# Kernel optimization log

Hardware: AMD Instinct MI355X
Metric: run time of the kernel (lower is better)

The kernel has to match this reference:

```python
import jax, jax.numpy as jnp
import numpy as np
import math

N_HEADS, INPUT_DIM, EMBED_DIM = 8, 512, 512
KEY_DIM = EMBED_DIM // N_HEADS  # val_dim == key_dim == 64
B, NQ, G = 4, 2048, 2048


def setup_inputs() -> dict:
    key = jax.random.key(0)
    ks = jax.random.split(key, 7)
    stdv_k = 1.0 / math.sqrt(KEY_DIM)
    stdv_e = 1.0 / math.sqrt(EMBED_DIM)
    return {
        "q": jax.random.normal(ks[0], (B, NQ, INPUT_DIM), jnp.float32),
        "h": jax.random.normal(ks[1], (B, G, INPUT_DIM), jnp.float32),
        "mask": jax.random.randint(ks[2], (B, NQ, G), 0, 2) == 1,  # True = attention not possible
        "W_query": jax.random.uniform(ks[3], (N_HEADS, INPUT_DIM, KEY_DIM), jnp.float32, -stdv_k, stdv_k),
        "W_key": jax.random.uniform(ks[4], (N_HEADS, INPUT_DIM, KEY_DIM), jnp.float32, -stdv_k, stdv_k),
        "W_val": jax.random.uniform(ks[5], (N_HEADS, INPUT_DIM, KEY_DIM), jnp.float32, -stdv_k, stdv_k),
        "W_out": jax.random.uniform(ks[6], (N_HEADS, KEY_DIM, EMBED_DIM), jnp.float32, -stdv_e, stdv_e),
    }


def reference(q, h, mask, W_query, W_key, W_val, W_out):
    norm = 1.0 / math.sqrt(KEY_DIM)
    # Per-head projections: (H, B, S, kd)
    Q = jnp.einsum("bqd,hdk->hbqk", q, W_query)
    K = jnp.einsum("bgd,hdk->hbgk", h, W_key)
    V = jnp.einsum("bgd,hdv->hbgv", h, W_val)
    # Full attention scores: (H, B, NQ, G)
    comp = norm * jnp.einsum("hbqk,hbgk->hbqg", Q, K)
    m = mask[None]  # (1, B, NQ, G) broadcasts over heads
    comp = jnp.where(m, -jnp.inf, comp)
    attn = jax.nn.softmax(comp, axis=-1)
    attn = jnp.where(m, 0.0, attn)  # mirrors the clone + zero step (also fixes all-masked rows)
    heads = jnp.einsum("hbqg,hbgv->hbqv", attn, V)
    # Output projection: flatten heads and apply W_out (H, vd, E)
    out = jnp.einsum("hbqv,hve->bqe", heads, W_out)
    return out
```

## Files before the change

### kernel.cpp

```cpp
#include <hip/hip_runtime.h>
#include <hip/hip_bf16.h>
#include <stdint.h>

#define NHEADS 8
#define INDIM 512
#define EMB 512
#define BSZ 4
#define NQS 2048
#define GS 2048

#define ALPHA_F 0.18033688011112042f

#if __has_builtin(__builtin_amdgcn_exp2f)
#define EXP2(x) __builtin_amdgcn_exp2f(x)
#else
#define EXP2(x) __expf((x)*0.69314718056f)
#endif

typedef short bf16x8 __attribute__((ext_vector_type(8)));
typedef float f32x4 __attribute__((ext_vector_type(4)));
typedef float f32x16 __attribute__((ext_vector_type(16)));
typedef unsigned int u32x4 __attribute__((ext_vector_type(4)));

static __device__ __forceinline__ unsigned short f2bf(float f) {
  unsigned int u = __builtin_bit_cast(unsigned int, f);
  unsigned int rounding = 0x7FFFu + ((u >> 16) & 1u);
  u += rounding;
  return (unsigned short)(u >> 16);
}

typedef __attribute__((address_space(3))) void lds_void;
typedef __attribute__((address_space(1))) const void gm_void;
static __device__ __forceinline__ void gll16(const void* g, void* s) {
  __builtin_amdgcn_global_load_lds((gm_void*)g, (lds_void*)s, 16, 0, 0);
}

__global__ void k_prep(const float4* __restrict__ q, const float4* __restrict__ h,
                       const void* __restrict__ mask,
                       const float* __restrict__ wq, const float* __restrict__ wk,
                       const float* __restrict__ wv, const float* __restrict__ wo,
                       ushort4* __restrict__ qb, ushort4* __restrict__ hb,
                       unsigned short* __restrict__ wqt, unsigned short* __restrict__ wkvt,
                       unsigned short* __restrict__ wot, unsigned short* __restrict__ maskB16) {
  int blk = blockIdx.x, t = threadIdx.x;
  if (blk < 2048) {
    const float4* src = blk < 1024 ? q : h;
    ushort4* dst = blk < 1024 ? qb : hb;
    int base = (blk & 1023) * 256 + t;
#pragma unroll
    for (int i = 0; i < 4; i++) {
      int idx = base + i * 262144;
      float4 v = src[idx];
      ushort4 o;
      o.x = f2bf(v.x); o.y = f2bf(v.y); o.z = f2bf(v.z); o.w = f2bf(v.w);
      dst[idx] = o;
    }
  } else if (blk < 3072) {
    const unsigned int* m32h = (const unsigned int*)mask;
    bool bytes = __ballot(m32h[t & 63] > 1u) != 0ull;
    int base = (blk - 2048) * 256 + t;
#pragma unroll
    for (int i = 0; i < 4; i++) {
      int widx = base + i * 262144;
      unsigned int bits = 0;
      if (bytes) {
        const uchar4* p = (const uchar4*)((const unsigned char*)mask + (size_t)widx * 16);
#pragma unroll
        for (int j = 0; j < 4; j++) {
          uchar4 v = p[j];
          bits |= ((v.x ? 1u : 0u) << (4 * j)) | ((v.y ? 1u : 0u) << (4 * j + 1)) |
                  ((v.z ? 1u : 0u) << (4 * j + 2)) | ((v.w ? 1u : 0u) << (4 * j + 3));
        }
      } else {
        const int4* p = (const int4*)((const int*)mask + (size_t)widx * 16);
#pragma unroll
        for (int j = 0; j < 4; j++) {
          int4 v = p[j];
          bits |= ((v.x ? 1u : 0u) << (4 * j)) | ((v.y ? 1u : 0u) << (4 * j + 1)) |
                  ((v.z ? 1u : 0u) << (4 * j + 2)) | ((v.w ? 1u : 0u) << (4 * j + 3));
        }
      }
      maskB16[widx] = (unsigned short)bits;
    }
  } else {
    int id = (blk - 3072) * 256 + t;
#pragma unroll
    for (int i = 0; i < 8; i++) {
      int e = id * 8 + i;
      int which = e >> 18, r = e & 262143;
      int k = r & 511, n = r >> 9;
      int hh = n >> 6, j = n & 63;
      if (which == 0) wqt[r] = f2bf(wq[hh * 32768 + k * 64 + j] * ALPHA_F);
      else if (which == 1) wkvt[r] = f2bf(wk[hh * 32768 + k * 64 + j]);
      else if (which == 2) wkvt[262144 + r] = f2bf(wv[hh * 32768 + k * 64 + j]);
      else wot[r] = f2bf(wo[k * 512 + n]);
    }
  }
}

template <int MODE>
__global__ __launch_bounds__(256) void k_gemm3(const unsigned short* __restrict__ A,
                                               const unsigned short* __restrict__ Bt,
                                               void* __restrict__ C, void* __restrict__ C2) {
  __shared__ unsigned short As[2][4096];
  __shared__ unsigned short Bs[2][8192];
  int m0 = blockIdx.x * 64, n0 = blockIdx.y * 128;
  int t = threadIdx.x;
  int w = t >> 6, l = t & 63, c = l & 15, lg = l >> 4;
  int wr = w >> 1, wc = w & 1;

  int rbA = t >> 7, kcc = (t >> 4) & 7, cc = t & 15;
  const unsigned short* aG = A + (size_t)(m0 + rbA * 16 + cc) * 512 + kcc * 8;
  const unsigned short* bG = Bt + (size_t)(n0 + rbA * 16 + cc) * 512 + kcc * 8;
  int ldsOff = w * 1024 + (t & 63) * 16;

  f32x4 acc[2][4];
#pragma unroll
  for (int mi = 0; mi < 2; mi++)
#pragma unroll
    for (int ni = 0; ni < 4; ni++) acc[mi][ni] = {0.f, 0.f, 0.f, 0.f};

  gll16(aG, (char*)As[0] + ldsOff);
  gll16(aG + 32 * 512, (char*)As[0] + ldsOff + 4096);
  gll16(bG, (char*)Bs[0] + ldsOff);
  gll16(bG + 32 * 512, (char*)Bs[0] + ldsOff + 4096);
  gll16(bG + 64 * 512, (char*)Bs[0] + ldsOff + 8192);
  gll16(bG + 96 * 512, (char*)Bs[0] + ldsOff + 12288);

  for (int kk = 0; kk < 8; kk++) {
    int cur = kk & 1;
    asm volatile("s_waitcnt vmcnt(0)" ::: "memory");
    __builtin_amdgcn_s_barrier();
    if (kk < 7) {
      int ko = (kk + 1) * 64;
      gll16(aG + ko, (char*)As[cur ^ 1] + ldsOff);
      gll16(aG + ko + 32 * 512, (char*)As[cur ^ 1] + ldsOff + 4096);
      gll16(bG + ko, (char*)Bs[cur ^ 1] + ldsOff);
      gll16(bG + ko + 32 * 512, (char*)Bs[cur ^ 1] + ldsOff + 4096);
      gll16(bG + ko + 64 * 512, (char*)Bs[cur ^ 1] + ldsOff + 8192);
      gll16(bG + ko + 96 * 512, (char*)Bs[cur ^ 1] + ldsOff + 12288);
    }
    bf16x8 af[2][2], bfr[4][2];
#pragma unroll
    for (int kc = 0; kc < 2; kc++) {
#pragma unroll
      for (int mi = 0; mi < 2; mi++)
        af[mi][kc] = *(const bf16x8*)((const char*)As[cur] + ((wr * 2 + mi) * 128 + (kc * 4 + lg) * 16 + c) * 16);
#pragma unroll
      for (int ni = 0; ni < 4; ni++)
        bfr[ni][kc] = *(const bf16x8*)((const char*)Bs[cur] + ((wc * 4 + ni) * 128 + (kc * 4 + lg) * 16 + c) * 16);
    }
#pragma unroll
    for (int kc = 0; kc < 2; kc++)
#pragma unroll
      for (int mi = 0; mi < 2; mi++)
#pragma unroll
        for (int ni = 0; ni < 4; ni++)
          acc[mi][ni] = __builtin_amdgcn_mfma_f32_16x16x32_bf16(af[mi][kc], bfr[ni][kc], acc[mi][ni], 0, 0, 0);
  }

#pragma unroll
  for (int mi = 0; mi < 2; mi++)
#pragma unroll
    for (int ni = 0; ni < 4; ni++) {
      int row = m0 + wr * 32 + mi * 16 + 4 * lg;
      int col = n0 + wc * 64 + ni * 16 + c;
#pragma unroll
      for (int r = 0; r < 4; r++)
        ((float*)C)[(size_t)(row + r) * 512 + col] = acc[mi][ni][r];
    }
}

__global__ __launch_bounds__(256) void k_gemmQKV(const unsigned short* __restrict__ qb_,
                                                 const unsigned short* __restrict__ hb_,
                                                 const unsigned short* __restrict__ wqt,
                                                 const unsigned short* __restrict__ wkvt,
                                                 unsigned short* __restrict__ Qp,
                                                 unsigned short* __restrict__ Kp,
                                                 unsigned short* __restrict__ Vt) {
  __shared__ unsigned short As[2][4096];
  __shared__ unsigned short Bs[2][8192];
  int ny = blockIdx.y;
  const unsigned short* A = (ny < 4) ? qb_ : hb_;
  const unsigned short* Bt = (ny < 4) ? wqt : wkvt;
  int n0 = (ny < 4) ? ny * 128 : (ny - 4) * 128;
  int m0 = blockIdx.x * 64;
  int t = threadIdx.x;
  int w = t >> 6, l = t & 63, c = l & 15, lg = l >> 4;
  int wr = w >> 1, wc = w & 1;

  int rbA = t >> 7, kcc = (t >> 4) & 7, cc = t & 15;
  const unsigned short* aG = A + (size_t)(m0 + rbA * 16 + cc) * 512 + kcc * 8;
  const unsigned short* bG = Bt + (size_t)(n0 + rbA * 16 + cc) * 512 + kcc * 8;
  int ldsOff = w * 1024 + (t & 63) * 16;

  f32x4 acc[2][4];
#pragma unroll
  for (int mi = 0; mi < 2; mi++)
#pragma unroll
    for (int ni = 0; ni < 4; ni++) acc[mi][ni] = {0.f, 0.f, 0.f, 0.f};

  gll16(aG, (char*)As[0] + ldsOff);
  gll16(aG + 32 * 512, (char*)As[0] + ldsOff + 4096);
  gll16(bG, (char*)Bs[0] + ldsOff);
  gll16(bG + 32 * 512, (char*)Bs[0] + ldsOff + 4096);
  gll16(bG + 64 * 512, (char*)Bs[0] + ldsOff + 8192);
  gll16(bG + 96 * 512, (char*)Bs[0] + ldsOff + 12288);

  for (int kk = 0; kk < 8; kk++) {
    int cur = kk & 1;
    asm volatile("s_waitcnt vmcnt(0)" ::: "memory");
    __builtin_amdgcn_s_barrier();
    if (kk < 7) {
      int ko = (kk + 1) * 64;
      gll16(aG + ko, (char*)As[cur ^ 1] + ldsOff);
      gll16(aG + ko + 32 * 512, (char*)As[cur ^ 1] + ldsOff + 4096);
      gll16(bG + ko, (char*)Bs[cur ^ 1] + ldsOff);
      gll16(bG + ko + 32 * 512, (char*)Bs[cur ^ 1] + ldsOff + 4096);
      gll16(bG + ko + 64 * 512, (char*)Bs[cur ^ 1] + ldsOff + 8192);
      gll16(bG + ko + 96 * 512, (char*)Bs[cur ^ 1] + ldsOff + 12288);
    }
    bf16x8 af[2][2], bfr[4][2];
#pragma unroll
    for (int kc = 0; kc < 2; kc++) {
#pragma unroll
      for (int mi = 0; mi < 2; mi++)
        af[mi][kc] = *(const bf16x8*)((const char*)As[cur] + ((wr * 2 + mi) * 128 + (kc * 4 + lg) * 16 + c) * 16);
#pragma unroll
      for (int ni = 0; ni < 4; ni++)
        bfr[ni][kc] = *(const bf16x8*)((const char*)Bs[cur] + ((wc * 4 + ni) * 128 + (kc * 4 + lg) * 16 + c) * 16);
    }
#pragma unroll
    for (int kc = 0; kc < 2; kc++)
#pragma unroll
      for (int mi = 0; mi < 2; mi++)
#pragma unroll
        for (int ni = 0; ni < 4; ni++)
          acc[mi][ni] = __builtin_amdgcn_mfma_f32_16x16x32_bf16(af[mi][kc], bfr[ni][kc], acc[mi][ni], 0, 0, 0);
  }

#pragma unroll
  for (int mi = 0; mi < 2; mi++)
#pragma unroll
    for (int ni = 0; ni < 4; ni++) {
      int row = m0 + wr * 32 + mi * 16 + 4 * lg;
      int col = n0 + wc * 64 + ni * 16 + c;
      if (ny < 4) {
#pragma unroll
        for (int r = 0; r < 4; r++)
          Qp[(size_t)(row + r) * 512 + col] = f2bf(acc[mi][ni][r]);
      } else if (col < 512) {
#pragma unroll
        for (int r = 0; r < 4; r++)
          Kp[(size_t)(row + r) * 512 + col] = f2bf(acc[mi][ni][r]);
      } else {
        int col5 = col - 512, hd2 = col5 >> 6, vv = col5 & 63;
        int bb = row >> 11, g = row & 2047;
        ushort4 u;
        u.x = f2bf(acc[mi][ni][0]);
        u.y = f2bf(acc[mi][ni][1]);
        u.z = f2bf(acc[mi][ni][2]);
        u.w = f2bf(acc[mi][ni][3]);
        *(ushort4*)(Vt + (size_t)((bb * 8 + hd2) * 64 + vv) * GS + g) = u;
      }
    }
}

__global__ __launch_bounds__(256, 2) void k_attn8(const unsigned short* __restrict__ Qp,
                                                  const unsigned short* __restrict__ Kp,
                                                  const unsigned short* __restrict__ Vt,
                                                  const unsigned short* __restrict__ maskB16,
                                                  unsigned short* __restrict__ Hd) {
  __shared__ unsigned short Ksh[2][4096];
  __shared__ unsigned short Vsh[2][4096];

  int bid = blockIdx.x;
  int fid = (bid & 7) * 64 + (bid >> 3);
  int qtile = fid & 15;
  int bh = fid >> 4;
  int b = bh >> 3, hd = bh & 7;

  int t = threadIdx.x;
  int w = t >> 6, l = t & 63;
  int lo = l & 31, hi = l >> 5, hi4 = hi * 4;
  int q = qtile * 128 + w * 32 + lo;

  const unsigned short* qrow = Qp + (size_t)(b * NQS + q) * 512 + hd * 64 + hi * 8;
  bf16x8 qf[4];
#pragma unroll
  for (int s = 0; s < 4; s++) qf[s] = *(const bf16x8*)(qrow + s * 16);

  const unsigned short* kg0 = Kp + (size_t)(b * GS + lo) * 512 + hd * 64 + w * 16 + hi * 8;
  int vbS = (t >> 7) & 1, s2S = (t >> 6) & 1;
  const unsigned short* vg0 = Vt + (size_t)(bh * 64 + vbS * 32 + lo) * GS + s2S * 16 + hi * 8;
  char* kd[2] = {(char*)Ksh[0] + w * 1024, (char*)Ksh[1] + w * 1024};
  char* vd[2] = {(char*)Vsh[0] + w * 1024, (char*)Vsh[1] + w * 1024};

  f32x16 o0, o1;
#pragma unroll
  for (int i = 0; i < 16; i++) { o0[i] = 0.f; o1[i] = 0.f; }
  float ls[4] = {0.f, 0.f, 0.f, 0.f};

  const unsigned long long* mrow = (const unsigned long long*)maskB16 + (size_t)(b * NQS + q) * 32;

  gll16(kg0, kd[0]);
  gll16(kg0 + 32 * 512, kd[0] + 4096);
  gll16(vg0, vd[0]);
  gll16(vg0 + 32, vd[0] + 4096);
  unsigned long long wm = mrow[0], wmn = 0;

  for (int kt = 0; kt < 32; kt++) {
    int cur = kt & 1;
    asm volatile("s_waitcnt vmcnt(0)" ::: "memory");
    __builtin_amdgcn_s_barrier();
    if (kt < 31) {
      const unsigned short* kg = kg0 + (size_t)(kt + 1) * 64 * 512;
      const unsigned short* vg = vg0 + (size_t)(kt + 1) * 64;
      gll16(kg, kd[cur ^ 1]);
      gll16(kg + 32 * 512, kd[cur ^ 1] + 4096);
      gll16(vg, vd[cur ^ 1]);
      gll16(vg + 32, vd[cur ^ 1] + 4096);
      wmn = mrow[kt + 1];
    }

#pragma unroll
    for (int g2 = 0; g2 < 2; g2++) {
      const unsigned short* Kc = (const unsigned short*)Ksh[cur] + g2 * 2048;
      f32x16 sreg;
#pragma unroll
      for (int i = 0; i < 16; i++) sreg[i] = 0.f;
      __builtin_amdgcn_s_setprio(1);
#pragma unroll
      for (int s = 0; s < 4; s++) {
        bf16x8 ka = *(const bf16x8*)(Kc + (s * 64 + l) * 8);
        sreg = __builtin_amdgcn_mfma_f32_32x32x16_bf16(ka, qf[s], sreg, 0, 0, 0);
      }
      __builtin_amdgcn_s_setprio(0);
      unsigned int mbits = (unsigned int)(wm >> (g2 * 32));
      float p[16];
#pragma unroll
      for (int r = 0; r < 16; r++) {
        float e = EXP2(sreg[r]);
        unsigned bit = (mbits >> ((r & 3) + 8 * (r >> 2) + hi4)) & 1u;
        p[r] = bit ? 0.f : e;
        ls[r & 3] += p[r];
      }
      unsigned int cw0, cw1, cw2, cw3, cw4, cw5, cw6, cw7;
      asm("v_cvt_pk_bf16_f32 %0, %1, %2" : "=v"(cw0) : "v"(p[0]), "v"(p[1]));
      asm("v_cvt_pk_bf16_f32 %0, %1, %2" : "=v"(cw1) : "v"(p[2]), "v"(p[3]));
      asm("v_cvt_pk_bf16_f32 %0, %1, %2" : "=v"(cw2) : "v"(p[4]), "v"(p[5]));
      asm("v_cvt_pk_bf16_f32 %0, %1, %2" : "=v"(cw3) : "v"(p[6]), "v"(p[7]));
      asm("v_cvt_pk_bf16_f32 %0, %1, %2" : "=v"(cw4) : "v"(p[8]), "v"(p[9]));
      asm("v_cvt_pk_bf16_f32 %0, %1, %2" : "=v"(cw5) : "v"(p[10]), "v"(p[11]));
      asm("v_cvt_pk_bf16_f32 %0, %1, %2" : "=v"(cw6) : "v"(p[12]), "v"(p[13]));
      asm("v_cvt_pk_bf16_f32 %0, %1, %2" : "=v"(cw7) : "v"(p[14]), "v"(p[15]));
      asm("v_permlane32_swap_b32 %0, %1" : "+v"(cw0), "+v"(cw2));
      asm("v_permlane32_swap_b32 %0, %1" : "+v"(cw1), "+v"(cw3));
      asm("v_permlane32_swap_b32 %0, %1" : "+v"(cw4), "+v"(cw6));
      asm("v_permlane32_swap_b32 %0, %1" : "+v"(cw5), "+v"(cw7));
      u32x4 pw0 = {cw0, cw1, cw2, cw3};
      u32x4 pw1 = {cw4, cw5, cw6, cw7};
      bf16x8 pb0 = __builtin_bit_cast(bf16x8, pw0);
      bf16x8 pb1 = __builtin_bit_cast(bf16x8, pw1);
      const unsigned short* Vc = (const unsigned short*)Vsh[cur] + g2 * 2048;
      bf16x8 va00 = *(const bf16x8*)(Vc + (0 * 64 + l) * 8);
      bf16x8 va01 = *(const bf16x8*)(Vc + (1 * 64 + l) * 8);
      bf16x8 va10 = *(const bf16x8*)(Vc + (2 * 64 + l) * 8);
      bf16x8 va11 = *(const bf16x8*)(Vc + (3 * 64 + l) * 8);
      __builtin_amdgcn_s_setprio(1);
      o0 = __builtin_amdgcn_mfma_f32_32x32x16_bf16(va00, pb0, o0, 0, 0, 0);
      o1 = __builtin_amdgcn_mfma_f32_32x32x16_bf16(va10, pb0, o1, 0, 0, 0);
      o0 = __builtin_amdgcn_mfma_f32_32x32x16_bf16(va01, pb1, o0, 0, 0, 0);
      o1 = __builtin_amdgcn_mfma_f32_32x32x16_bf16(va11, pb1, o1, 0, 0, 0);
      __builtin_amdgcn_s_setprio(0);
    }
    wm = wmn;
  }

  float lsum = (ls[0] + ls[1]) + (ls[2] + ls[3]);
  lsum += __shfl_xor(lsum, 32);
  float inv = lsum > 0.f ? 1.0f / lsum : 0.f;
  unsigned short* hrow = Hd + (size_t)(b * NQS + q) * 512 + hd * 64;
#pragma unroll
  for (int vt = 0; vt < 2; vt++) {
#pragma unroll
    for (int gr = 0; gr < 4; gr++) {
      ushort4 u;
      float v0 = (vt ? o1[gr * 4 + 0] : o0[gr * 4 + 0]) * inv;
      float v1 = (vt ? o1[gr * 4 + 1] : o0[gr * 4 + 1]) * inv;
      float v2 = (vt ? o1[gr * 4 + 2] : o0[gr * 4 + 2]) * inv;
      float v3 = (vt ? o1[gr * 4 + 3] : o0[gr * 4 + 3]) * inv;
      u.x = f2bf(v0); u.y = f2bf(v1); u.z = f2bf(v2); u.w = f2bf(v3);
      int vv = vt * 32 + 8 * gr + hi4;
      *(ushort4*)(hrow + vv) = u;
    }
  }
}


extern "C" void kernel_launch(void* const* d_in, const int* in_sizes, int n_in,
                              void* d_out, int out_size, void* d_ws, size_t ws_size,
                              hipStream_t stream) {
  const float* q = (const float*)d_in[0];
  const float* h = (const float*)d_in[1];
  const void* mask = d_in[2];
  const float* wq = (const float*)d_in[3];
  const float* wk = (const float*)d_in[4];
  const float* wv = (const float*)d_in[5];
  const float* wo = (const float*)d_in[6];
  float* out = (float*)d_out;

  unsigned short* qb_ = (unsigned short*)d_ws;
  unsigned short* hb_ = qb_ + 8192 * 512;
  unsigned short* Qp = hb_ + 8192 * 512;
  unsigned short* Kp = Qp + 8192 * 512;
  unsigned short* Vtp = Kp + 8192 * 512;
  unsigned short* Hd = Vtp + 8192 * 512;
  unsigned short* wqt = Hd + 8192 * 512;
  unsigned short* wkvt = wqt + 512 * 512;
  unsigned short* wot = wkvt + 1024 * 512;
  unsigned short* maskB16 = wot + 512 * 512;

  k_prep<<<3584, 256, 0, stream>>>((const float4*)q, (const float4*)h, mask, wq, wk, wv, wo,
                                   (ushort4*)qb_, (ushort4*)hb_, wqt, wkvt, wot, maskB16);
  dim3 gqkv(128, 12);
  k_gemmQKV<<<gqkv, 256, 0, stream>>>(qb_, hb_, wqt, wkvt, Qp, Kp, Vtp);
  k_attn8<<<512, 256, 0, stream>>>(Qp, Kp, Vtp, maskB16, Hd);
  dim3 go(128, 4);
  k_gemm3<1><<<go, 256, 0, stream>>>(Hd, wot, out, nullptr);
}
```

Baseline: 143.3 us.

## Split attention over key halves and combine partial outputs in a separate kernel

The attention kernel now splits the key/value sequence into two halves, so it launches twice as many blocks. Each block writes an unnormalized partial output and a partial row-sum, and a new combine kernel adds the two halves and normalizes. The launch-bounds occupancy hint rises from 2 to 4 blocks, aiming for more resident waves to hide latency. The cost is an extra launch, extra global traffic for the partials, and an additional bf16 rounding of the partial outputs.

Result: no change. 145.6 us (+1.6%).

```diff
diff --git a/kernel.cpp b/kernel.cpp
--- a/kernel.cpp
+++ b/kernel.cpp
@@ -27,6 +27,9 @@
   unsigned int rounding = 0x7FFFu + ((u >> 16) & 1u);
   u += rounding;
   return (unsigned short)(u >> 16);
+}
+static __device__ __forceinline__ float bfbits2f(unsigned int hi16bits) {
+  return __builtin_bit_cast(float, hi16bits);
 }
 
 typedef __attribute__((address_space(3))) void lds_void;
@@ -266,24 +269,27 @@
     }
 }
 
-__global__ __launch_bounds__(256, 2) void k_attn8(const unsigned short* __restrict__ Qp,
+__global__ __launch_bounds__(256, 4) void k_attn9(const unsigned short* __restrict__ Qp,
                                                   const unsigned short* __restrict__ Kp,
                                                   const unsigned short* __restrict__ Vt,
                                                   const unsigned short* __restrict__ maskB16,
-                                                  unsigned short* __restrict__ Hd) {
+                                                  unsigned short* __restrict__ Op,
+                                                  float* __restrict__ Lp) {
   __shared__ unsigned short Ksh[2][4096];
   __shared__ unsigned short Vsh[2][4096];
 
   int bid = blockIdx.x;
-  int fid = (bid & 7) * 64 + (bid >> 3);
+  int fid = (bid & 7) * 128 + (bid >> 3);
   int qtile = fid & 15;
-  int bh = fid >> 4;
+  int half = (fid >> 4) & 1;
+  int bh = fid >> 5;
   int b = bh >> 3, hd = bh & 7;
 
   int t = threadIdx.x;
   int w = t >> 6, l = t & 63;
   int lo = l & 31, hi = l >> 5, hi4 = hi * 4;
   int q = qtile * 128 + w * 32 + lo;
+  int kt0 = half * 16;
 
   const unsigned short* qrow = Qp + (size_t)(b * NQS + q) * 512 + hd * 64 + hi * 8;
   bf16x8 qf[4];
@@ -303,17 +309,18 @@
 
   const unsigned long long* mrow = (const unsigned long long*)maskB16 + (size_t)(b * NQS + q) * 32;
 
-  gll16(kg0, kd[0]);
-  gll16(kg0 + 32 * 512, kd[0] + 4096);
-  gll16(vg0, vd[0]);
-  gll16(vg0 + 32, vd[0] + 4096);
-  unsigned long long wm = mrow[0], wmn = 0;
-
-  for (int kt = 0; kt < 32; kt++) {
-    int cur = kt & 1;
+  gll16(kg0 + (size_t)kt0 * 64 * 512, kd[0]);
+  gll16(kg0 + (size_t)kt0 * 64 * 512 + 32 * 512, kd[0] + 4096);
+  gll16(vg0 + (size_t)kt0 * 64, vd[0]);
+  gll16(vg0 + (size_t)kt0 * 64 + 32, vd[0] + 4096);
+  unsigned long long wm = mrow[kt0], wmn = 0;
+
+  for (int ki = 0; ki < 16; ki++) {
+    int kt = kt0 + ki;
+    int cur = ki & 1;
     asm volatile("s_waitcnt vmcnt(0)" ::: "memory");
     __builtin_amdgcn_s_barrier();
-    if (kt < 31) {
+    if (ki < 15) {
       const unsigned short* kg = kg0 + (size_t)(kt + 1) * 64 * 512;
       const unsigned short* vg = vg0 + (size_t)(kt + 1) * 64;
       gll16(kg, kd[cur ^ 1]);
@@ -379,22 +386,49 @@
 
   float lsum = (ls[0] + ls[1]) + (ls[2] + ls[3]);
   lsum += __shfl_xor(lsum, 32);
-  float inv = lsum > 0.f ? 1.0f / lsum : 0.f;
-  unsigned short* hrow = Hd + (size_t)(b * NQS + q) * 512 + hd * 64;
+  size_t qidx = (size_t)(b * NQS + q);
+  if (hi == 0) Lp[(size_t)half * 65536 + qidx * 8 + hd] = lsum;
+  unsigned short* orow = Op + (size_t)half * 8192 * 512 + qidx * 512 + hd * 64;
 #pragma unroll
   for (int vt = 0; vt < 2; vt++) {
 #pragma unroll
     for (int gr = 0; gr < 4; gr++) {
       ushort4 u;
-      float v0 = (vt ? o1[gr * 4 + 0] : o0[gr * 4 + 0]) * inv;
-      float v1 = (vt ? o1[gr * 4 + 1] : o0[gr * 4 + 1]) * inv;
-      float v2 = (vt ? o1[gr * 4 + 2] : o0[gr * 4 + 2]) * inv;
-      float v3 = (vt ? o1[gr * 4 + 3] : o0[gr * 4 + 3]) * inv;
+      float v0 = (vt ? o1[gr * 4 + 0] : o0[gr * 4 + 0]);
+      float v1 = (vt ? o1[gr * 4 + 1] : o0[gr * 4 + 1]);
+      float v2 = (vt ? o1[gr * 4 + 2] : o0[gr * 4 + 2]);
+      float v3 = (vt ? o1[gr * 4 + 3] : o0[gr * 4 + 3]);
       u.x = f2bf(v0); u.y = f2bf(v1); u.z = f2bf(v2); u.w = f2bf(v3);
       int vv = vt * 32 + 8 * gr + hi4;
-      *(ushort4*)(hrow + vv) = u;
-    }
-  }
+      *(ushort4*)(orow + vv) = u;
+    }
+  }
+}
+
+__global__ void k_comb(const unsigned short* __restrict__ Op, const float* __restrict__ Lp,
+                       unsigned short* __restrict__ Hd) {
+  size_t i = (size_t)blockIdx.x * 256 + threadIdx.x;
+  size_t base = i * 8;
+  int qi = (int)(base >> 9);
+  int hd = (int)((base >> 6) & 7);
+  float lt = Lp[(size_t)qi * 8 + hd] + Lp[65536 + (size_t)qi * 8 + hd];
+  float inv = lt > 0.f ? 1.0f / lt : 0.f;
+  uint4 a = *(const uint4*)(Op + base);
+  uint4 bq = *(const uint4*)(Op + (size_t)8192 * 512 + base);
+  unsigned int wa[4] = {a.x, a.y, a.z, a.w};
+  unsigned int wb[4] = {bq.x, bq.y, bq.z, bq.w};
+  uint4 outw;
+  unsigned int ow[4];
+#pragma unroll
+  for (int j = 0; j < 4; j++) {
+    float f0 = bfbits2f(wa[j] << 16) + bfbits2f(wb[j] << 16);
+    float f1 = bfbits2f(wa[j] & 0xffff0000u) + bfbits2f(wb[j] & 0xffff0000u);
+    unsigned int r;
+    asm("v_cvt_pk_bf16_f32 %0, %1, %2" : "=v"(r) : "v"(f0 * inv), "v"(f1 * inv));
+    ow[j] = r;
+  }
+  outw.x = ow[0]; outw.y = ow[1]; outw.z = ow[2]; outw.w = ow[3];
+  *(uint4*)(Hd + base) = outw;
 }
 
 
@@ -420,12 +454,14 @@
   unsigned short* wkvt = wqt + 512 * 512;
   unsigned short* wot = wkvt + 1024 * 512;
   unsigned short* maskB16 = wot + 512 * 512;
+  float* Lp = (float*)(maskB16 + (size_t)4 * 2048 * 128);
 
   k_prep<<<3584, 256, 0, stream>>>((const float4*)q, (const float4*)h, mask, wq, wk, wv, wo,
                                    (ushort4*)qb_, (ushort4*)hb_, wqt, wkvt, wot, maskB16);
   dim3 gqkv(128, 12);
   k_gemmQKV<<<gqkv, 256, 0, stream>>>(qb_, hb_, wqt, wkvt, Qp, Kp, Vtp);
-  k_attn8<<<512, 256, 0, stream>>>(Qp, Kp, Vtp, maskB16, Hd);
+  k_attn9<<<1024, 256, 0, stream>>>(Qp, Kp, Vtp, maskB16, qb_, Lp);
+  k_comb<<<2048, 256, 0, stream>>>(qb_, Lp, Hd);
   dim3 go(128, 4);
   k_gemm3<1><<<go, 256, 0, stream>>>(Hd, wot, out, nullptr);
 }
```
